# Kernel optimization log

Hardware: AMD Instinct MI355X
Metric: run time of the kernel (lower is better)

The kernel has to match this reference:

```python
import jax, jax.numpy as jnp
import numpy as np

TOP_K = 2          # n_activated_experts
ROUTE_SCALE = 1.0  # args.route_scale


def setup_inputs() -> dict:
    key = jax.random.key(0)
    ks = jax.random.split(key, 12)
    B, S, D, I, E = 8, 2048, 512, 1024, 8
    SH = 2 * I  # n_shared_experts * moe_inter_dim
    std = 0.02
    return {
        "x": jax.random.normal(ks[0], (B, S, D), jnp.float32),
        "gate_w": (jax.random.normal(ks[1], (E, D), jnp.float32) * std),
        "w1": (jax.random.normal(ks[2], (E, D, I), jnp.float32) * std),
        "w2": (jax.random.normal(ks[3], (E, I, D), jnp.float32) * std),
        "w3": (jax.random.normal(ks[4], (E, D, I), jnp.float32) * std),
        "sw1": (jax.random.normal(ks[5], (D, SH), jnp.float32) * std),
        "sb1": jnp.zeros((SH,), jnp.float32),
        "sw2": (jax.random.normal(ks[6], (SH, D), jnp.float32) * std),
        "sb2": jnp.zeros((D,), jnp.float32),
        "sw3": (jax.random.normal(ks[7], (D, SH), jnp.float32) * std),
        "sb3": jnp.zeros((SH,), jnp.float32),
    }


def reference(x, gate_w, w1, w2, w3, sw1, sb1, sw2, sb2, sw3, sb3):
    B, S, D = x.shape
    xt = x.reshape(-1, D)              # [T, D] tokens
    T = xt.shape[0]
    E = gate_w.shape[0]

    # --- Gate: sigmoid scores, top-k, renormalized weights ---
    scores = jax.nn.sigmoid(xt @ gate_w.T)                 # [T, E]
    topv, topi = jax.lax.top_k(scores, TOP_K)              # [T, K]
    wts = topv / jnp.sum(topv, axis=-1, keepdims=True)
    wts = wts * ROUTE_SCALE

    # Dense combine weights: zero for non-selected experts -> faithful to
    # the torch masked scatter-accumulate over the expert loop.
    cw = jnp.zeros((T, E), xt.dtype).at[jnp.arange(T)[:, None], topi].add(wts)

    # --- Routed SwiGLU experts (ffn_bias=False) ---
    y = jnp.zeros_like(xt)
    for e in range(E):  # fixed small structural loop over experts
        h = jax.nn.silu(xt @ w1[e]) * (xt @ w3[e])         # [T, I]
        y = y + cw[:, e:e + 1] * (h @ w2[e])               # combine

    # --- Load-balance aux loss L_ExpBal ---
    counts = jnp.zeros((E,), xt.dtype).at[topi.reshape(-1)].add(1.0)
    f_i = E * counts / (TOP_K * T)
    P_i = cw.sum(axis=0) / T   # per-expert sum of routed weights
    L_ExpBal = jnp.sum(f_i * P_i)

    # --- Shared experts MLP (biased Linear, SwiGLU) ---
    z = (jax.nn.silu(xt @ sw1 + sb1) * (xt @ sw3 + sb3)) @ sw2 + sb2

    return (y + z).reshape(B, S, D), L_ExpBal
```

## Files before the change

kernel.cpp:

```cpp
#include <hip/hip_runtime.h>
#include <math.h>
#include <stdint.h>

#define T_TOK 16384
#define DDIM  512
#define IDIM  1024
#define NEXP  8
#define SHDIM 2048
#define MT_R  264
#define MPAD  (MT_R * 128)
#define GBLK  256

typedef unsigned short u16;
typedef short bf16x8 __attribute__((ext_vector_type(8)));
typedef float f32x4 __attribute__((ext_vector_type(4)));

__device__ __forceinline__ u16 f2bf(float f) {
    unsigned u = __float_as_uint(f);
    u += 0x7FFF + ((u >> 16) & 1);
    return (u16)(u >> 16);
}
__device__ __forceinline__ float bf2f(u16 h) {
    return __uint_as_float((unsigned)h << 16);
}

__device__ __forceinline__ void gload_lds16(const void* g, void* l) {
    __builtin_amdgcn_global_load_lds(
        (const __attribute__((address_space(1))) void*)g,
        (__attribute__((address_space(3))) void*)l, 16, 0, 0);
}

__device__ __forceinline__ int xcd_swz(int id, int nwg) {
    return (id & 7) * (nwg >> 3) + (id >> 3);
}

__global__ void k_zero(int* cursors) {
    int i = threadIdx.x;
    if (i < NEXP) cursors[i] = 0;
}

__global__ __launch_bounds__(256) void k_gate(
    const float* __restrict__ x, const float* __restrict__ gw,
    int* __restrict__ topi, float* __restrict__ wts,
    int* __restrict__ pcnt, float* __restrict__ pps, u16* __restrict__ xb)
{
    __shared__ int   cnt[NEXP];
    __shared__ float ps[NEXP];
    const int tid = threadIdx.x;
    if (tid < NEXP) { cnt[tid] = 0; ps[tid] = 0.f; }
    __syncthreads();
    const int wid = tid >> 6, lane = tid & 63;

    const float4* gw4 = (const float4*)gw;
    float4 g0[NEXP], g1[NEXP];
#pragma unroll
    for (int e = 0; e < NEXP; e++) {
        g0[e] = gw4[e * 128 + lane];
        g1[e] = gw4[e * 128 + 64 + lane];
    }

    const int t0 = blockIdx.x * 64 + wid * 16;
    for (int u = 0; u < 16; u++) {
        int t = t0 + u;
        const float4* xr4 = (const float4*)(x + (size_t)t * DDIM);
        float4 v0 = xr4[lane];
        float4 v1 = xr4[64 + lane];
        ushort4 o0 = { f2bf(v0.x), f2bf(v0.y), f2bf(v0.z), f2bf(v0.w) };
        ushort4 o1 = { f2bf(v1.x), f2bf(v1.y), f2bf(v1.z), f2bf(v1.w) };
        ushort4* xbo = (ushort4*)(xb + (size_t)t * DDIM);
        xbo[lane] = o0;
        xbo[64 + lane] = o1;
        float acc[NEXP];
#pragma unroll
        for (int e = 0; e < NEXP; e++) {
            acc[e] = v0.x * g0[e].x + v0.y * g0[e].y + v0.z * g0[e].z + v0.w * g0[e].w
                   + v1.x * g1[e].x + v1.y * g1[e].y + v1.z * g1[e].z + v1.w * g1[e].w;
        }
#pragma unroll
        for (int e = 0; e < NEXP; e++) {
#pragma unroll
            for (int off = 32; off; off >>= 1) acc[e] += __shfl_xor(acc[e], off, 64);
        }
        if (lane == 0) {
            float s[NEXP];
#pragma unroll
            for (int e = 0; e < NEXP; e++) s[e] = 1.f / (1.f + expf(-acc[e]));
            int i1 = 0; float v1s = s[0];
#pragma unroll
            for (int e = 1; e < NEXP; e++) if (s[e] > v1s) { v1s = s[e]; i1 = e; }
            int i2 = -1; float v2s = -1.f;
#pragma unroll
            for (int e = 0; e < NEXP; e++) if (e != i1 && s[e] > v2s) { v2s = s[e]; i2 = e; }
            float inv = 1.f / (v1s + v2s);
            float wa = v1s * inv, wb = v2s * inv;
            topi[2 * t] = i1; topi[2 * t + 1] = i2;
            wts[2 * t] = wa;  wts[2 * t + 1] = wb;
            atomicAdd(&cnt[i1], 1); atomicAdd(&cnt[i2], 1);
            atomicAdd(&ps[i1], wa); atomicAdd(&ps[i2], wb);
        }
    }
    __syncthreads();
    if (tid < NEXP) {
        pcnt[blockIdx.x * NEXP + tid] = cnt[tid];
        pps[blockIdx.x * NEXP + tid]  = ps[tid];
    }
}

__global__ void k_scan(const int* __restrict__ pcnt, const float* __restrict__ pps,
                       int* __restrict__ off_pad, float* __restrict__ out_loss)
{
    __shared__ int   scnt[8][NEXP];
    __shared__ float sps[8][NEXP];
    int tid = threadIdx.x;
    if (tid < 64) {
        int e = tid & 7, part = tid >> 3;
        int c = 0; float p = 0.f;
        for (int b = part * 32; b < part * 32 + 32; b++) {
            c += pcnt[b * NEXP + e];
            p += pps[b * NEXP + e];
        }
        scnt[part][e] = c; sps[part][e] = p;
    }
    __syncthreads();
    if (tid == 0) {
        int off = 0; float L = 0.f;
        for (int e = 0; e < NEXP; e++) {
            int c = 0; float p = 0.f;
            for (int q = 0; q < 8; q++) { c += scnt[q][e]; p += sps[q][e]; }
            off_pad[e] = off;
            off += (c + 127) & ~127;
            float f = (float)NEXP * (float)c / (float)(2 * T_TOK);
            L += f * (p / (float)T_TOK);
        }
        off_pad[NEXP] = off;
        out_loss[0] = L;
    }
}

__global__ void k_fillperm(int* __restrict__ perm) {
    int i = blockIdx.x * blockDim.x + threadIdx.x;
    if (i < MPAD) perm[i] = -1;
}

__global__ __launch_bounds__(256) void k_scatter(
    const int* __restrict__ topi, const float* __restrict__ wts,
    const int* __restrict__ off_pad, int* __restrict__ cursors,
    int* __restrict__ perm, float* __restrict__ pw, int* __restrict__ inv)
{
    __shared__ int lcnt[NEXP];
    __shared__ int lbase[NEXP];
    int tid = threadIdx.x;
    if (tid < NEXP) lcnt[tid] = 0;
    __syncthreads();
    int t = blockIdx.x * 256 + tid;
    int e0 = topi[2 * t], e1 = topi[2 * t + 1];
    int p0 = atomicAdd(&lcnt[e0], 1);
    int p1 = atomicAdd(&lcnt[e1], 1);
    __syncthreads();
    if (tid < NEXP) lbase[tid] = atomicAdd(&cursors[tid], lcnt[tid]);
    __syncthreads();
    int s0 = off_pad[e0] + lbase[e0] + p0;
    int s1 = off_pad[e1] + lbase[e1] + p1;
    perm[s0] = t; pw[s0] = wts[2 * t];
    perm[s1] = t; pw[s1] = wts[2 * t + 1];
    inv[2 * t] = s0; inv[2 * t + 1] = s1;
}

__global__ __launch_bounds__(256) void k_gather(const u16* __restrict__ xb,
                                                const int* __restrict__ perm,
                                                u16* __restrict__ xg) {
    int row = blockIdx.x * 2 + (threadIdx.x >> 7);
    int c = (threadIdx.x & 127) * 4;
    int tok = perm[row];
    ushort4 v = {0, 0, 0, 0};
    if (tok >= 0) v = *(const ushort4*)&xb[(size_t)tok * DDIM + c];
    *(ushort4*)&xg[(size_t)row * DDIM + c] = v;
}

__global__ __launch_bounds__(256) void k_transpose(const float* __restrict__ src,
                                                   u16* __restrict__ dst, int R, int C)
{
    __shared__ u16 t[64][68];
    const float* s = src + (size_t)blockIdx.z * R * C;
    u16* d = dst + (size_t)blockIdx.z * R * C;
    int r0 = blockIdx.y * 64, c0 = blockIdx.x * 64;
    int tid = threadIdx.x;
    int lr = tid >> 4, lc = (tid & 15) * 4;
#pragma unroll
    for (int u = 0; u < 4; u++) {
        int r = lr + u * 16;
        float4 v = *(const float4*)&s[(size_t)(r0 + r) * C + c0 + lc];
        t[lc + 0][r] = f2bf(v.x);
        t[lc + 1][r] = f2bf(v.y);
        t[lc + 2][r] = f2bf(v.z);
        t[lc + 3][r] = f2bf(v.w);
    }
    __syncthreads();
    int wr = tid >> 4, wc = (tid & 15) * 4;
#pragma unroll
    for (int u = 0; u < 4; u++) {
        int c = wr + u * 16;
        ushort4 o = { t[c][wc], t[c][wc + 1], t[c][wc + 2], t[c][wc + 3] };
        *(ushort4*)&d[(size_t)(c0 + c) * R + r0 + wc] = o;
    }
}

template<int K, bool ROUTED, bool BIAS>
__global__ __launch_bounds__(256, 2) void k_s1(
    const u16* __restrict__ A, const u16* __restrict__ B1t, const u16* __restrict__ B3t,
    const float* __restrict__ bias1, const float* __restrict__ bias3,
    u16* __restrict__ H, int ldh, const int* __restrict__ off_pad)
{
    __shared__ __align__(16) u16 sA[2][128 * 32], sB1[2][128 * 32], sB3[2][128 * 32];
    const int nwg = gridDim.x * gridDim.y;
    const int id  = xcd_swz(blockIdx.y * gridDim.x + blockIdx.x, nwg);
    const int m0 = (id / gridDim.x) * 128;
    const int n0 = (id % gridDim.x) * 128;
    if (ROUTED && m0 >= off_pad[NEXP]) return;
    const u16* b1 = B1t; const u16* b3 = B3t;
    if (ROUTED) {
        int e = 0;
        while (off_pad[e + 1] <= m0) e++;
        b1 += (size_t)e * IDIM * DDIM;
        b3 += (size_t)e * IDIM * DDIM;
    }
    const int tid = threadIdx.x;
    const int wid = tid >> 6, lane = tid & 63;
    const int srow = wid * 16 + (lane >> 2);
    const int skk  = (lane & 3) * 8;
    const u16* gA  = A  + (size_t)(m0 + srow) * K + skk;
    const u16* gB1 = b1 + (size_t)(n0 + srow) * K + skk;
    const u16* gB3 = b3 + (size_t)(n0 + srow) * K + skk;
    const int ldst = wid * 512;
    const int fr = lane & 15;
    const int fk = (lane >> 4) * 8;
    const int wrow = (wid >> 1) * 64, wcol = (wid & 1) * 64;

    f32x4 acc1[4][4], acc3[4][4];
#pragma unroll
    for (int i = 0; i < 4; i++)
#pragma unroll
        for (int j = 0; j < 4; j++) { acc1[i][j] = {0.f, 0.f, 0.f, 0.f}; acc3[i][j] = {0.f, 0.f, 0.f, 0.f}; }

#pragma unroll
    for (int p = 0; p < 2; p++) {
        gload_lds16(gA  + (size_t)p * 64 * K, &sA [0][ldst + p * 2048]);
        gload_lds16(gB1 + (size_t)p * 64 * K, &sB1[0][ldst + p * 2048]);
        gload_lds16(gB3 + (size_t)p * 64 * K, &sB3[0][ldst + p * 2048]);
    }
    __syncthreads();

    int cur = 0;
    for (int k0 = 0; k0 < K; k0 += 32) {
        if (k0 + 32 < K) {
#pragma unroll
            for (int p = 0; p < 2; p++) {
                gload_lds16(gA  + (size_t)p * 64 * K + k0 + 32, &sA [cur ^ 1][ldst + p * 2048]);
                gload_lds16(gB1 + (size_t)p * 64 * K + k0 + 32, &sB1[cur ^ 1][ldst + p * 2048]);
                gload_lds16(gB3 + (size_t)p * 64 * K + k0 + 32, &sB3[cur ^ 1][ldst + p * 2048]);
            }
        }
        bf16x8 av[4], b1v[4], b3v[4];
#pragma unroll
        for (int i = 0; i < 4; i++) {
            av[i]  = *(const bf16x8*)(&sA [cur][(wrow + i * 16 + fr) * 32 + fk]);
            b1v[i] = *(const bf16x8*)(&sB1[cur][(wcol + i * 16 + fr) * 32 + fk]);
            b3v[i] = *(const bf16x8*)(&sB3[cur][(wcol + i * 16 + fr) * 32 + fk]);
        }
#pragma unroll
        for (int i = 0; i < 4; i++)
#pragma unroll
            for (int j = 0; j < 4; j++) {
                acc1[i][j] = __builtin_amdgcn_mfma_f32_16x16x32_bf16(av[i], b1v[j], acc1[i][j], 0, 0, 0);
                acc3[i][j] = __builtin_amdgcn_mfma_f32_16x16x32_bf16(av[i], b3v[j], acc3[i][j], 0, 0, 0);
            }
        __syncthreads();
        cur ^= 1;
    }

    const int rr = (lane >> 4) * 4;
#pragma unroll
    for (int i = 0; i < 4; i++) {
#pragma unroll
        for (int j = 0; j < 4; j++) {
            int col = n0 + wcol + j * 16 + fr;
            float bb1 = BIAS ? bias1[col] : 0.f;
            float bb3 = BIAS ? bias3[col] : 0.f;
#pragma unroll
            for (int r = 0; r < 4; r++) {
                int row = m0 + wrow + i * 16 + rr + r;
                float v1 = acc1[i][j][r] + bb1;
                float v3 = acc3[i][j][r] + bb3;
                float hv = (v1 / (1.f + __expf(-v1))) * v3;
                H[(size_t)row * ldh + col] = f2bf(hv);
            }
        }
    }
}

template<int K, bool ROUTED>
__global__ __launch_bounds__(256, 2) void k_s2(
    const u16* __restrict__ A, const u16* __restrict__ Bt,
    const float* __restrict__ bias2, float* __restrict__ out,
    u16* __restrict__ ytmp, const int* __restrict__ off_pad)
{
    __shared__ __align__(16) u16 sA[2][128 * 32], sB[2][128 * 32];
    const int nwg = gridDim.x * gridDim.y;
    const int id  = xcd_swz(blockIdx.y * gridDim.x + blockIdx.x, nwg);
    const int m0 = (id / gridDim.x) * 128;
    const int n0 = (id % gridDim.x) * 128;
    if (ROUTED && m0 >= off_pad[NEXP]) return;
    const u16* bt = Bt;
    if (ROUTED) {
        int e = 0;
        while (off_pad[e + 1] <= m0) e++;
        bt += (size_t)e * DDIM * IDIM;
    }
    const int tid = threadIdx.x;
    const int wid = tid >> 6, lane = tid & 63;
    const int srow = wid * 16 + (lane >> 2);
    const int skk  = (lane & 3) * 8;
    const u16* gA = A  + (size_t)(m0 + srow) * K + skk;
    const u16* gB = bt + (size_t)(n0 + srow) * K + skk;
    const int ldst = wid * 512;
    const int fr = lane & 15;
    const int fk = (lane >> 4) * 8;
    const int wrow = (wid >> 1) * 64, wcol = (wid & 1) * 64;

    f32x4 acc[4][4];
#pragma unroll
    for (int i = 0; i < 4; i++)
#pragma unroll
        for (int j = 0; j < 4; j++) acc[i][j] = {0.f, 0.f, 0.f, 0.f};

#pragma unroll
    for (int p = 0; p < 2; p++) {
        gload_lds16(gA + (size_t)p * 64 * K, &sA[0][ldst + p * 2048]);
        gload_lds16(gB + (size_t)p * 64 * K, &sB[0][ldst + p * 2048]);
    }
    __syncthreads();

    int cur = 0;
    for (int k0 = 0; k0 < K; k0 += 32) {
        if (k0 + 32 < K) {
#pragma unroll
            for (int p = 0; p < 2; p++) {
                gload_lds16(gA + (size_t)p * 64 * K + k0 + 32, &sA[cur ^ 1][ldst + p * 2048]);
                gload_lds16(gB + (size_t)p * 64 * K + k0 + 32, &sB[cur ^ 1][ldst + p * 2048]);
            }
        }
        bf16x8 av[4], bv[4];
#pragma unroll
        for (int i = 0; i < 4; i++) {
            av[i] = *(const bf16x8*)(&sA[cur][(wrow + i * 16 + fr) * 32 + fk]);
            bv[i] = *(const bf16x8*)(&sB[cur][(wcol + i * 16 + fr) * 32 + fk]);
        }
#pragma unroll
        for (int i = 0; i < 4; i++)
#pragma unroll
            for (int j = 0; j < 4; j++)
                acc[i][j] = __builtin_amdgcn_mfma_f32_16x16x32_bf16(av[i], bv[j], acc[i][j], 0, 0, 0);
        __syncthreads();
        cur ^= 1;
    }

    const int rr = (lane >> 4) * 4;
#pragma unroll
    for (int i = 0; i < 4; i++) {
#pragma unroll
        for (int r = 0; r < 4; r++) {
            int row = m0 + wrow + i * 16 + rr + r;
#pragma unroll
            for (int j = 0; j < 4; j++) {
                int col = n0 + wcol + j * 16 + fr;
                float v = acc[i][j][r];
                if (ROUTED) {
                    ytmp[(size_t)row * DDIM + col] = f2bf(v);
                } else {
                    out[(size_t)row * DDIM + col] = v + bias2[col];
                }
            }
        }
    }
}

__global__ __launch_bounds__(256) void k_combine(
    const u16* __restrict__ ytmp, const int* __restrict__ inv,
    const float* __restrict__ wts, float* __restrict__ out)
{
    int idx = blockIdx.x * 256 + threadIdx.x;
    int t = idx >> 7;
    int c = (idx & 127) * 4;
    int s0 = inv[2 * t], s1 = inv[2 * t + 1];
    float w0 = wts[2 * t], w1 = wts[2 * t + 1];
    ushort4 a = *(const ushort4*)&ytmp[(size_t)s0 * DDIM + c];
    ushort4 b = *(const ushort4*)&ytmp[(size_t)s1 * DDIM + c];
    float4 o = *(float4*)&out[(size_t)t * DDIM + c];
    o.x += w0 * bf2f(a.x) + w1 * bf2f(b.x);
    o.y += w0 * bf2f(a.y) + w1 * bf2f(b.y);
    o.z += w0 * bf2f(a.z) + w1 * bf2f(b.z);
    o.w += w0 * bf2f(a.w) + w1 * bf2f(b.w);
    *(float4*)&out[(size_t)t * DDIM + c] = o;
}

extern "C" void kernel_launch(void* const* d_in, const int* in_sizes, int n_in,
                              void* d_out, int out_size, void* d_ws, size_t ws_size,
                              hipStream_t stream)
{
    const float* x   = (const float*)d_in[0];
    const float* gw  = (const float*)d_in[1];
    const float* w1  = (const float*)d_in[2];
    const float* w2  = (const float*)d_in[3];
    const float* w3  = (const float*)d_in[4];
    const float* sw1 = (const float*)d_in[5];
    const float* sb1 = (const float*)d_in[6];
    const float* sw2 = (const float*)d_in[7];
    const float* sb2 = (const float*)d_in[8];
    const float* sw3 = (const float*)d_in[9];
    const float* sb3 = (const float*)d_in[10];
    float* out = (float*)d_out;

    char* ws = (char*)d_ws;
    size_t off = 0;
    int*   topi    = (int*)(ws + off);   off += (size_t)2 * T_TOK * 4;
    float* wts     = (float*)(ws + off); off += (size_t)2 * T_TOK * 4;
    int*   perm    = (int*)(ws + off);   off += (size_t)MPAD * 4;
    float* pw      = (float*)(ws + off); off += (size_t)MPAD * 4;
    int*   cursors = (int*)(ws + off);   off += 256;
    int*   off_pad = (int*)(ws + off);   off += 256;
    int*   pcnt    = (int*)(ws + off);   off += (size_t)GBLK * NEXP * 4;
    float* pps     = (float*)(ws + off); off += (size_t)GBLK * NEXP * 4;
    int*   inv     = (int*)(ws + off);   off += (size_t)2 * T_TOK * 4;
    u16*   xb      = (u16*)(ws + off);   off += (size_t)T_TOK * DDIM * 2;
    u16*   xg      = (u16*)(ws + off);   off += (size_t)MPAD * DDIM * 2;
    u16*   w1T     = (u16*)(ws + off);   off += (size_t)NEXP * IDIM * DDIM * 2;
    u16*   w3T     = (u16*)(ws + off);   off += (size_t)NEXP * IDIM * DDIM * 2;
    u16*   w2T     = (u16*)(ws + off);   off += (size_t)NEXP * DDIM * IDIM * 2;
    u16*   sw1T    = (u16*)(ws + off);   off += (size_t)SHDIM * DDIM * 2;
    u16*   sw3T    = (u16*)(ws + off);   off += (size_t)SHDIM * DDIM * 2;
    u16*   sw2T    = (u16*)(ws + off);   off += (size_t)DDIM * SHDIM * 2;
    u16*   hb      = (u16*)(ws + off);   off += (size_t)MPAD * IDIM * 2;
    u16*   ytmp    = xg;

    k_zero<<<1, 64, 0, stream>>>(cursors);
    k_gate<<<GBLK, 256, 0, stream>>>(x, gw, topi, wts, pcnt, pps, xb);
    k_scan<<<1, 64, 0, stream>>>(pcnt, pps, off_pad, out + (size_t)T_TOK * DDIM);
    k_fillperm<<<(MPAD + 255) / 256, 256, 0, stream>>>(perm);
    k_scatter<<<T_TOK / 256, 256, 0, stream>>>(topi, wts, off_pad, cursors, perm, pw, inv);

    k_gather<<<MPAD / 2, 256, 0, stream>>>(xb, perm, xg);
    k_transpose<<<dim3(IDIM / 64, DDIM / 64, NEXP), 256, 0, stream>>>(w1, w1T, DDIM, IDIM);
    k_transpose<<<dim3(IDIM / 64, DDIM / 64, NEXP), 256, 0, stream>>>(w3, w3T, DDIM, IDIM);
    k_transpose<<<dim3(DDIM / 64, IDIM / 64, NEXP), 256, 0, stream>>>(w2, w2T, IDIM, DDIM);
    k_transpose<<<dim3(SHDIM / 64, DDIM / 64, 1), 256, 0, stream>>>(sw1, sw1T, DDIM, SHDIM);
    k_transpose<<<dim3(SHDIM / 64, DDIM / 64, 1), 256, 0, stream>>>(sw3, sw3T, DDIM, SHDIM);
    k_transpose<<<dim3(DDIM / 64, SHDIM / 64, 1), 256, 0, stream>>>(sw2, sw2T, SHDIM, DDIM);

    k_s1<DDIM, false, true><<<dim3(SHDIM / 128, T_TOK / 128), 256, 0, stream>>>(
        xb, sw1T, sw3T, sb1, sb3, hb, SHDIM, nullptr);
    k_s2<SHDIM, false><<<dim3(DDIM / 128, T_TOK / 128), 256, 0, stream>>>(
        hb, sw2T, sb2, out, nullptr, nullptr);
    k_s1<DDIM, true, false><<<dim3(IDIM / 128, MT_R), 256, 0, stream>>>(
        xg, w1T, w3T, nullptr, nullptr, hb, IDIM, off_pad);
    k_s2<IDIM, true><<<dim3(DDIM / 128, MT_R), 256, 0, stream>>>(
        hb, w2T, nullptr, nullptr, ytmp, off_pad);
    k_combine<<<(T_TOK * DDIM / 4) / 256, 256, 0, stream>>>(ytmp, inv, wts, out);
}
```

Baseline: 387.2 us.

## Drop LDS staging in GEMMs, fuse gather into routed GEMM, widen down-proj tiles

Both GEMM kernels stop staging tiles through LDS with barriers. Each lane now loads its MFMA fragments straight from global memory into registers, double-buffered. The routed gate/up GEMM reads token rows indirectly through perm, with a zero pad row for padding, which removes the separate gather kernel and the xg buffer. The down-projection tiles widen to 128x256, and the cursor zeroing moves into the scan kernel so one launch disappears. The aim is to cut barrier overhead, LDS traffic and launch count, at the cost of uncoalesced direct global loads, more register pressure, and redundant fragment loads that rely on L2 for reuse.

```diff
diff --git a/kernel.cpp b/kernel.cpp
--- a/kernel.cpp
+++ b/kernel.cpp
@@ -15,6 +15,8 @@
 typedef short bf16x8 __attribute__((ext_vector_type(8)));
 typedef float f32x4 __attribute__((ext_vector_type(4)));
 
+#define MFMA16(a, b, c) __builtin_amdgcn_mfma_f32_16x16x32_bf16((a), (b), (c), 0, 0, 0)
+
 __device__ __forceinline__ u16 f2bf(float f) {
     unsigned u = __float_as_uint(f);
     u += 0x7FFF + ((u >> 16) & 1);
@@ -24,19 +26,8 @@
     return __uint_as_float((unsigned)h << 16);
 }
 
-__device__ __forceinline__ void gload_lds16(const void* g, void* l) {
-    __builtin_amdgcn_global_load_lds(
-        (const __attribute__((address_space(1))) void*)g,
-        (__attribute__((address_space(3))) void*)l, 16, 0, 0);
-}
-
 __device__ __forceinline__ int xcd_swz(int id, int nwg) {
     return (id & 7) * (nwg >> 3) + (id >> 3);
-}
-
-__global__ void k_zero(int* cursors) {
-    int i = threadIdx.x;
-    if (i < NEXP) cursors[i] = 0;
 }
 
 __global__ __launch_bounds__(256) void k_gate(
@@ -107,11 +98,13 @@
 }
 
 __global__ void k_scan(const int* __restrict__ pcnt, const float* __restrict__ pps,
-                       int* __restrict__ off_pad, float* __restrict__ out_loss)
+                       int* __restrict__ off_pad, float* __restrict__ out_loss,
+                       int* __restrict__ cursors)
 {
     __shared__ int   scnt[8][NEXP];
     __shared__ float sps[8][NEXP];
     int tid = threadIdx.x;
+    if (tid < NEXP) cursors[tid] = 0;
     if (tid < 64) {
         int e = tid & 7, part = tid >> 3;
         int c = 0; float p = 0.f;
@@ -137,9 +130,10 @@
     }
 }
 
-__global__ void k_fillperm(int* __restrict__ perm) {
+__global__ void k_fillperm(int* __restrict__ perm, u16* __restrict__ zpad) {
     int i = blockIdx.x * blockDim.x + threadIdx.x;
     if (i < MPAD) perm[i] = -1;
+    if (blockIdx.x == 0 && threadIdx.x < 256) ((unsigned*)zpad)[threadIdx.x] = 0u;
 }
 
 __global__ __launch_bounds__(256) void k_scatter(
@@ -164,17 +158,6 @@
     perm[s0] = t; pw[s0] = wts[2 * t];
     perm[s1] = t; pw[s1] = wts[2 * t + 1];
     inv[2 * t] = s0; inv[2 * t + 1] = s1;
-}
-
-__global__ __launch_bounds__(256) void k_gather(const u16* __restrict__ xb,
-                                                const int* __restrict__ perm,
-                                                u16* __restrict__ xg) {
-    int row = blockIdx.x * 2 + (threadIdx.x >> 7);
-    int c = (threadIdx.x & 127) * 4;
-    int tok = perm[row];
-    ushort4 v = {0, 0, 0, 0};
-    if (tok >= 0) v = *(const ushort4*)&xb[(size_t)tok * DDIM + c];
-    *(ushort4*)&xg[(size_t)row * DDIM + c] = v;
 }
 
 __global__ __launch_bounds__(256) void k_transpose(const float* __restrict__ src,
@@ -205,17 +188,18 @@
     }
 }
 
-template<int K, bool ROUTED, bool BIAS>
-__global__ __launch_bounds__(256, 2) void k_s1(
-    const u16* __restrict__ A, const u16* __restrict__ B1t, const u16* __restrict__ B3t,
+
+template<bool ROUTED, bool BIAS, int GXB>
+__global__ __launch_bounds__(256, 2) void g_s1(
+    const u16* __restrict__ Axb, const u16* __restrict__ B1t, const u16* __restrict__ B3t,
     const float* __restrict__ bias1, const float* __restrict__ bias3,
-    u16* __restrict__ H, int ldh, const int* __restrict__ off_pad)
-{
-    __shared__ __align__(16) u16 sA[2][128 * 32], sB1[2][128 * 32], sB3[2][128 * 32];
-    const int nwg = gridDim.x * gridDim.y;
-    const int id  = xcd_swz(blockIdx.y * gridDim.x + blockIdx.x, nwg);
-    const int m0 = (id / gridDim.x) * 128;
-    const int n0 = (id % gridDim.x) * 128;
+    u16* __restrict__ H, int ldh, const int* __restrict__ off_pad,
+    const int* __restrict__ perm, const u16* __restrict__ zpad)
+{
+    const int nwg = GXB * gridDim.y;
+    const int id  = xcd_swz(blockIdx.y * GXB + blockIdx.x, nwg);
+    const int m0 = (id / GXB) * 128;
+    const int n0 = (id % GXB) * 128;
     if (ROUTED && m0 >= off_pad[NEXP]) return;
     const u16* b1 = B1t; const u16* b3 = B3t;
     if (ROUTED) {
@@ -224,17 +208,24 @@
         b1 += (size_t)e * IDIM * DDIM;
         b3 += (size_t)e * IDIM * DDIM;
     }
-    const int tid = threadIdx.x;
-    const int wid = tid >> 6, lane = tid & 63;
-    const int srow = wid * 16 + (lane >> 2);
-    const int skk  = (lane & 3) * 8;
-    const u16* gA  = A  + (size_t)(m0 + srow) * K + skk;
-    const u16* gB1 = b1 + (size_t)(n0 + srow) * K + skk;
-    const u16* gB3 = b3 + (size_t)(n0 + srow) * K + skk;
-    const int ldst = wid * 512;
-    const int fr = lane & 15;
-    const int fk = (lane >> 4) * 8;
-    const int wrow = (wid >> 1) * 64, wcol = (wid & 1) * 64;
+    const int lane = threadIdx.x & 63, wid = threadIdx.x >> 6;
+    const int wm = wid >> 1, wn = wid & 1;
+    const int fr = lane & 15, hi = lane >> 4;
+
+    const u16* pa[4]; const u16* pb1[4]; const u16* pb3[4];
+#pragma unroll
+    for (int i = 0; i < 4; i++) {
+        int row = m0 + wm * 64 + i * 16 + fr;
+        if (ROUTED) {
+            int tok = perm[row];
+            pa[i] = (tok >= 0 ? Axb + (size_t)tok * DDIM : zpad) + hi * 8;
+        } else {
+            pa[i] = Axb + (size_t)row * DDIM + hi * 8;
+        }
+        int br = n0 + wn * 64 + i * 16 + fr;
+        pb1[i] = b1 + (size_t)br * DDIM + hi * 8;
+        pb3[i] = b3 + (size_t)br * DDIM + hi * 8;
+    }
 
     f32x4 acc1[4][4], acc3[4][4];
 #pragma unroll
@@ -242,53 +233,45 @@
 #pragma unroll
         for (int j = 0; j < 4; j++) { acc1[i][j] = {0.f, 0.f, 0.f, 0.f}; acc3[i][j] = {0.f, 0.f, 0.f, 0.f}; }
 
-#pragma unroll
-    for (int p = 0; p < 2; p++) {
-        gload_lds16(gA  + (size_t)p * 64 * K, &sA [0][ldst + p * 2048]);
-        gload_lds16(gB1 + (size_t)p * 64 * K, &sB1[0][ldst + p * 2048]);
-        gload_lds16(gB3 + (size_t)p * 64 * K, &sB3[0][ldst + p * 2048]);
-    }
-    __syncthreads();
-
-    int cur = 0;
-    for (int k0 = 0; k0 < K; k0 += 32) {
-        if (k0 + 32 < K) {
-#pragma unroll
-            for (int p = 0; p < 2; p++) {
-                gload_lds16(gA  + (size_t)p * 64 * K + k0 + 32, &sA [cur ^ 1][ldst + p * 2048]);
-                gload_lds16(gB1 + (size_t)p * 64 * K + k0 + 32, &sB1[cur ^ 1][ldst + p * 2048]);
-                gload_lds16(gB3 + (size_t)p * 64 * K + k0 + 32, &sB3[cur ^ 1][ldst + p * 2048]);
+    bf16x8 fa[2][4], fb1[2][4], fb3[2][4];
+#pragma unroll
+    for (int i = 0; i < 4; i++) {
+        fa[0][i]  = *(const bf16x8*)(pa[i]);
+        fb1[0][i] = *(const bf16x8*)(pb1[i]);
+        fb3[0][i] = *(const bf16x8*)(pb3[i]);
+    }
+    const int NT = DDIM / 32;
+#pragma unroll
+    for (int t = 0; t < NT; t++) {
+        const int cs = t & 1, ns = cs ^ 1;
+        if (t + 1 < NT) {
+            const int ko = (t + 1) * 32;
+#pragma unroll
+            for (int i = 0; i < 4; i++) {
+                fa[ns][i]  = *(const bf16x8*)(pa[i]  + ko);
+                fb1[ns][i] = *(const bf16x8*)(pb1[i] + ko);
+                fb3[ns][i] = *(const bf16x8*)(pb3[i] + ko);
             }
         }
-        bf16x8 av[4], b1v[4], b3v[4];
-#pragma unroll
-        for (int i = 0; i < 4; i++) {
-            av[i]  = *(const bf16x8*)(&sA [cur][(wrow + i * 16 + fr) * 32 + fk]);
-            b1v[i] = *(const bf16x8*)(&sB1[cur][(wcol + i * 16 + fr) * 32 + fk]);
-            b3v[i] = *(const bf16x8*)(&sB3[cur][(wcol + i * 16 + fr) * 32 + fk]);
-        }
 #pragma unroll
         for (int i = 0; i < 4; i++)
 #pragma unroll
             for (int j = 0; j < 4; j++) {
-                acc1[i][j] = __builtin_amdgcn_mfma_f32_16x16x32_bf16(av[i], b1v[j], acc1[i][j], 0, 0, 0);
-                acc3[i][j] = __builtin_amdgcn_mfma_f32_16x16x32_bf16(av[i], b3v[j], acc3[i][j], 0, 0, 0);
+                acc1[i][j] = MFMA16(fa[cs][i], fb1[cs][j], acc1[i][j]);
+                acc3[i][j] = MFMA16(fa[cs][i], fb3[cs][j], acc3[i][j]);
             }
-        __syncthreads();
-        cur ^= 1;
-    }
-
-    const int rr = (lane >> 4) * 4;
+    }
+
 #pragma unroll
     for (int i = 0; i < 4; i++) {
 #pragma unroll
         for (int j = 0; j < 4; j++) {
-            int col = n0 + wcol + j * 16 + fr;
+            int col = n0 + wn * 64 + j * 16 + fr;
             float bb1 = BIAS ? bias1[col] : 0.f;
             float bb3 = BIAS ? bias3[col] : 0.f;
 #pragma unroll
             for (int r = 0; r < 4; r++) {
-                int row = m0 + wrow + i * 16 + rr + r;
+                int row = m0 + wm * 64 + i * 16 + hi * 4 + r;
                 float v1 = acc1[i][j][r] + bb1;
                 float v3 = acc3[i][j][r] + bb3;
                 float hv = (v1 / (1.f + __expf(-v1))) * v3;
@@ -298,17 +281,17 @@
     }
 }
 
-template<int K, bool ROUTED>
-__global__ __launch_bounds__(256, 2) void k_s2(
+template<int K, int EPI, int GXB>
+__global__ __launch_bounds__(256, 2) void g_s2(
     const u16* __restrict__ A, const u16* __restrict__ Bt,
     const float* __restrict__ bias2, float* __restrict__ out,
     u16* __restrict__ ytmp, const int* __restrict__ off_pad)
 {
-    __shared__ __align__(16) u16 sA[2][128 * 32], sB[2][128 * 32];
-    const int nwg = gridDim.x * gridDim.y;
-    const int id  = xcd_swz(blockIdx.y * gridDim.x + blockIdx.x, nwg);
-    const int m0 = (id / gridDim.x) * 128;
-    const int n0 = (id % gridDim.x) * 128;
+    constexpr bool ROUTED = (EPI == 2);
+    const int nwg = GXB * gridDim.y;
+    const int id  = xcd_swz(blockIdx.y * GXB + blockIdx.x, nwg);
+    const int m0 = (id / GXB) * 128;
+    const int n0 = (id % GXB) * 256;
     if (ROUTED && m0 >= off_pad[NEXP]) return;
     const u16* bt = Bt;
     if (ROUTED) {
@@ -316,69 +299,79 @@
         while (off_pad[e + 1] <= m0) e++;
         bt += (size_t)e * DDIM * IDIM;
     }
-    const int tid = threadIdx.x;
-    const int wid = tid >> 6, lane = tid & 63;
-    const int srow = wid * 16 + (lane >> 2);
-    const int skk  = (lane & 3) * 8;
-    const u16* gA = A  + (size_t)(m0 + srow) * K + skk;
-    const u16* gB = bt + (size_t)(n0 + srow) * K + skk;
-    const int ldst = wid * 512;
-    const int fr = lane & 15;
-    const int fk = (lane >> 4) * 8;
-    const int wrow = (wid >> 1) * 64, wcol = (wid & 1) * 64;
-
-    f32x4 acc[4][4];
+    const int lane = threadIdx.x & 63, wid = threadIdx.x >> 6;
+    const int wm = wid >> 1, wn = wid & 1;
+    const int fr = lane & 15, hi = lane >> 4;
+
+    const u16* pa[4]; const u16* pb[8];
 #pragma unroll
     for (int i = 0; i < 4; i++)
-#pragma unroll
-        for (int j = 0; j < 4; j++) acc[i][j] = {0.f, 0.f, 0.f, 0.f};
-
-#pragma unroll
-    for (int p = 0; p < 2; p++) {
-        gload_lds16(gA + (size_t)p * 64 * K, &sA[0][ldst + p * 2048]);
-        gload_lds16(gB + (size_t)p * 64 * K, &sB[0][ldst + p * 2048]);
-    }
-    __syncthreads();
-
-    int cur = 0;
-    for (int k0 = 0; k0 < K; k0 += 32) {
-        if (k0 + 32 < K) {
-#pragma unroll
-            for (int p = 0; p < 2; p++) {
-                gload_lds16(gA + (size_t)p * 64 * K + k0 + 32, &sA[cur ^ 1][ldst + p * 2048]);
-                gload_lds16(gB + (size_t)p * 64 * K + k0 + 32, &sB[cur ^ 1][ldst + p * 2048]);
-            }
-        }
-        bf16x8 av[4], bv[4];
-#pragma unroll
-        for (int i = 0; i < 4; i++) {
-            av[i] = *(const bf16x8*)(&sA[cur][(wrow + i * 16 + fr) * 32 + fk]);
-            bv[i] = *(const bf16x8*)(&sB[cur][(wcol + i * 16 + fr) * 32 + fk]);
+        pa[i] = A + (size_t)(m0 + wm * 64 + i * 16 + fr) * K + hi * 8;
+#pragma unroll
+    for (int j = 0; j < 8; j++)
+        pb[j] = bt + (size_t)(n0 + wn * 128 + j * 16 + fr) * K + hi * 8;
+
+    f32x4 acc[4][8];
+#pragma unroll
+    for (int i = 0; i < 4; i++)
+#pragma unroll
+        for (int j = 0; j < 8; j++) acc[i][j] = {0.f, 0.f, 0.f, 0.f};
+
+    bf16x8 fa[2][4], fb[2][8];
+#pragma unroll
+    for (int i = 0; i < 4; i++) fa[0][i] = *(const bf16x8*)(pa[i]);
+#pragma unroll
+    for (int j = 0; j < 8; j++) fb[0][j] = *(const bf16x8*)(pb[j]);
+
+    const int NT = K / 32;
+    for (int kb = 0; kb < NT - 4; kb += 4) {
+#pragma unroll
+        for (int u = 0; u < 4; u++) {
+            const int cs = u & 1, ns = cs ^ 1;
+            const int ko = (u + 1) * 32;
+#pragma unroll
+            for (int i = 0; i < 4; i++) fa[ns][i] = *(const bf16x8*)(pa[i] + ko);
+#pragma unroll
+            for (int j = 0; j < 8; j++) fb[ns][j] = *(const bf16x8*)(pb[j] + ko);
+#pragma unroll
+            for (int i = 0; i < 4; i++)
+#pragma unroll
+                for (int j = 0; j < 8; j++)
+                    acc[i][j] = MFMA16(fa[cs][i], fb[cs][j], acc[i][j]);
+        }
+#pragma unroll
+        for (int i = 0; i < 4; i++) pa[i] += 128;
+#pragma unroll
+        for (int j = 0; j < 8; j++) pb[j] += 128;
+    }
+#pragma unroll
+    for (int u = 0; u < 4; u++) {
+        const int cs = u & 1, ns = cs ^ 1;
+        if (u < 3) {
+            const int ko = (u + 1) * 32;
+#pragma unroll
+            for (int i = 0; i < 4; i++) fa[ns][i] = *(const bf16x8*)(pa[i] + ko);
+#pragma unroll
+            for (int j = 0; j < 8; j++) fb[ns][j] = *(const bf16x8*)(pb[j] + ko);
         }
 #pragma unroll
         for (int i = 0; i < 4; i++)
 #pragma unroll
-            for (int j = 0; j < 4; j++)
-                acc[i][j] = __builtin_amdgcn_mfma_f32_16x16x32_bf16(av[i], bv[j], acc[i][j], 0, 0, 0);
-        __syncthreads();
-        cur ^= 1;
-    }
-
-    const int rr = (lane >> 4) * 4;
+            for (int j = 0; j < 8; j++)
+                acc[i][j] = MFMA16(fa[cs][i], fb[cs][j], acc[i][j]);
+    }
+
 #pragma unroll
     for (int i = 0; i < 4; i++) {
 #pragma unroll
         for (int r = 0; r < 4; r++) {
-            int row = m0 + wrow + i * 16 + rr + r;
-#pragma unroll
-            for (int j = 0; j < 4; j++) {
-                int col = n0 + wcol + j * 16 + fr;
+            int row = m0 + wm * 64 + i * 16 + hi * 4 + r;
+#pragma unroll
+            for (int j = 0; j < 8; j++) {
+                int col = n0 + wn * 128 + j * 16 + fr;
                 float v = acc[i][j][r];
-                if (ROUTED) {
-                    ytmp[(size_t)row * DDIM + col] = f2bf(v);
-                } else {
-                    out[(size_t)row * DDIM + col] = v + bias2[col];
-                }
+                if (EPI == 2) ytmp[(size_t)row * DDIM + col] = f2bf(v);
+                else          out[(size_t)row * DDIM + col] = v + bias2[col];
             }
         }
     }
@@ -431,8 +424,9 @@
     int*   pcnt    = (int*)(ws + off);   off += (size_t)GBLK * NEXP * 4;
     float* pps     = (float*)(ws + off); off += (size_t)GBLK * NEXP * 4;
     int*   inv     = (int*)(ws + off);   off += (size_t)2 * T_TOK * 4;
+    u16*   zpad    = (u16*)(ws + off);   off += 1024;
     u16*   xb      = (u16*)(ws + off);   off += (size_t)T_TOK * DDIM * 2;
-    u16*   xg      = (u16*)(ws + off);   off += (size_t)MPAD * DDIM * 2;
+    u16*   ytmp    = (u16*)(ws + off);   off += (size_t)MPAD * DDIM * 2;
     u16*   w1T     = (u16*)(ws + off);   off += (size_t)NEXP * IDIM * DDIM * 2;
     u16*   w3T     = (u16*)(ws + off);   off += (size_t)NEXP * IDIM * DDIM * 2;
     u16*   w2T     = (u16*)(ws + off);   off += (size_t)NEXP * DDIM * IDIM * 2;
@@ -440,15 +434,12 @@
     u16*   sw3T    = (u16*)(ws + off);   off += (size_t)SHDIM * DDIM * 2;
     u16*   sw2T    = (u16*)(ws + off);   off += (size_t)DDIM * SHDIM * 2;
     u16*   hb      = (u16*)(ws + off);   off += (size_t)MPAD * IDIM * 2;
-    u16*   ytmp    = xg;
-
-    k_zero<<<1, 64, 0, stream>>>(cursors);
+
     k_gate<<<GBLK, 256, 0, stream>>>(x, gw, topi, wts, pcnt, pps, xb);
-    k_scan<<<1, 64, 0, stream>>>(pcnt, pps, off_pad, out + (size_t)T_TOK * DDIM);
-    k_fillperm<<<(MPAD + 255) / 256, 256, 0, stream>>>(perm);
+    k_scan<<<1, 64, 0, stream>>>(pcnt, pps, off_pad, out + (size_t)T_TOK * DDIM, cursors);
+    k_fillperm<<<MPAD / 256, 256, 0, stream>>>(perm, zpad);
     k_scatter<<<T_TOK / 256, 256, 0, stream>>>(topi, wts, off_pad, cursors, perm, pw, inv);
 
-    k_gather<<<MPAD / 2, 256, 0, stream>>>(xb, perm, xg);
     k_transpose<<<dim3(IDIM / 64, DDIM / 64, NEXP), 256, 0, stream>>>(w1, w1T, DDIM, IDIM);
     k_transpose<<<dim3(IDIM / 64, DDIM / 64, NEXP), 256, 0, stream>>>(w3, w3T, DDIM, IDIM);
     k_transpose<<<dim3(DDIM / 64, IDIM / 64, NEXP), 256, 0, stream>>>(w2, w2T, IDIM, DDIM);
@@ -456,13 +447,13 @@
     k_transpose<<<dim3(SHDIM / 64, DDIM / 64, 1), 256, 0, stream>>>(sw3, sw3T, DDIM, SHDIM);
     k_transpose<<<dim3(DDIM / 64, SHDIM / 64, 1), 256, 0, stream>>>(sw2, sw2T, SHDIM, DDIM);
 
-    k_s1<DDIM, false, true><<<dim3(SHDIM / 128, T_TOK / 128), 256, 0, stream>>>(
-        xb, sw1T, sw3T, sb1, sb3, hb, SHDIM, nullptr);
-    k_s2<SHDIM, false><<<dim3(DDIM / 128, T_TOK / 128), 256, 0, stream>>>(
-        hb, sw2T, sb2, out, nullptr, nullptr);
-    k_s1<DDIM, true, false><<<dim3(IDIM / 128, MT_R), 256, 0, stream>>>(
-        xg, w1T, w3T, nullptr, nullptr, hb, IDIM, off_pad);
-    k_s2<IDIM, true><<<dim3(DDIM / 128, MT_R), 256, 0, stream>>>(
+    g_s1<false, true, SHDIM / 128><<<dim3(SHDIM / 128, T_TOK / 128), 256, 0, stream>>>(
+        xb, sw1T, sw3T, sb1, sb3, hb, SHDIM, off_pad, nullptr, nullptr);
+    g_s2<SHDIM, 1, DDIM / 256><<<dim3(DDIM / 256, T_TOK / 128), 256, 0, stream>>>(
+        hb, sw2T, sb2, out, nullptr, off_pad);
+    g_s1<true, false, IDIM / 128><<<dim3(IDIM / 128, MT_R), 256, 0, stream>>>(
+        xb, w1T, w3T, nullptr, nullptr, hb, IDIM, off_pad, perm, zpad);
+    g_s2<IDIM, 2, DDIM / 256><<<dim3(DDIM / 256, MT_R), 256, 0, stream>>>(
         hb, w2T, nullptr, nullptr, ytmp, off_pad);
     k_combine<<<(T_TOK * DDIM / 4) / 256, 256, 0, stream>>>(ytmp, inv, wts, out);
 }
```

After: 730.1 us. +88.6%, slower.
